# Optimization experiments

Measured on AMD Instinct MI355X. Metric: run time of the kernel, lower is better.

Reference implementation:

```python
import jax, jax.numpy as jnp
import numpy as np

B, S, D, H, F = 64, 512, 512, 512, 8
G = 4 * H // F  # 256, rows of left Kronecker factors


def setup_inputs() -> dict:
    key = jax.random.key(0)
    ks = jax.random.split(key, 24)

    def n(k, shape, s=0.05):
        return jax.random.normal(k, shape, jnp.float32) * s

    return {
        "x": jax.random.normal(ks[0], (B, S, D), jnp.float32),
        "h0": jnp.zeros((2, B, H), jnp.float32),
        "c0": jnp.zeros((2, B, H), jnp.float32),
        # layer 1 (input dim D)
        "W11": n(ks[1], (G, 1)), "W12": n(ks[2], (F, D)),
        "U11": n(ks[3], (G, 1)), "U12": n(ks[4], (F, H)),
        "dW11": n(ks[5], (G, 1)), "dW12": n(ks[6], (F, D)),
        "dU11": n(ks[7], (G, 1)), "dU12": n(ks[8], (F, H)),
        "b11": n(ks[9], (4 * H, 1)), "b12": n(ks[10], (4 * H, 1)),
        # layer 2 (input dim H; init_weights reshapes W22 to (F, H))
        "W21": n(ks[11], (G, 1)), "W22": n(ks[12], (F, H)),
        "U21": n(ks[13], (G, 1)), "U22": n(ks[14], (F, H)),
        "dW21": n(ks[15], (G, 1)), "dW22": n(ks[16], (F, H)),
        "dU21": n(ks[17], (G, 1)), "dU22": n(ks[18], (F, H)),
        "b21": n(ks[19], (4 * H, 1)), "b22": n(ks[20], (4 * H, 1)),
    }


def _kron_col(a, M):
    # kron of column vector a:(G,1) with M:(F,B) -> (G*F, B) = (4H, B)
    return (a[:, :, None] * M[None, :, :]).reshape(a.shape[0] * M.shape[0], M.shape[1])


def _cell(xt, ht, ct, p):
    # xt:(B,Din) ht,ct:(B,H); gates computed as (4H,B) like the torch code
    W1, W2, U1, U2, dW1, dW2, dU1, dU2, b1, b2 = p
    g = (_kron_col(W1, W2 @ xt.T) + _kron_col(dW1, dW2 @ xt.T)
         + _kron_col(U1, U2 @ ht.T) + _kron_col(dU1, dU2 @ ht.T)
         + b1 + b2)
    i = jax.nn.sigmoid(g[:H])
    f = jax.nn.sigmoid(g[H:2 * H])
    gg = jnp.tanh(g[2 * H:3 * H])
    o = jax.nn.sigmoid(g[3 * H:])
    c = f * ct.T + i * gg            # (H,B)
    h = o * jnp.tanh(c)              # (H,B)
    return h.T, c.T                  # (B,H)


def reference(x, h0, c0,
              W11, W12, U11, U12, dW11, dW12, dU11, dU12, b11, b12,
              W21, W22, U21, U22, dW21, dW22, dU21, dU22, b21, b22):
    layers = [
        (W11, W12, U11, U12, dW11, dW12, dU11, dU12, b11, b12),
        (W21, W22, U21, U22, dW21, dW22, dU21, dU22, b21, b22),
    ]

    def step(carry, xt):
        h, c = carry  # each (2,B,H)
        inp = xt
        hs, cs = [], []
        for li in range(2):
            hn, cn = _cell(inp, h[li], c[li], layers[li])
            hs.append(hn)
            cs.append(cn)
            inp = hn
        return (jnp.stack(hs), jnp.stack(cs)), inp

    (hn, cn), seq = jax.lax.scan(step, (h0, c0), jnp.swapaxes(x, 0, 1))
    hidden_seq = jnp.swapaxes(seq, 0, 1)  # (B,S,H)
    return hidden_seq, hn, cn
```

## Files before the change

### kernel.cpp

```cpp
#include <hip/hip_runtime.h>
#include <math.h>

#define NB 64
#define NS 512
#define ND 512
#define NH 512
#define L2E 1.4426950408889634f

__device__ __forceinline__ float dpp_sum64(float x) {
    x += __int_as_float(__builtin_amdgcn_update_dpp(0, __float_as_int(x), 0x111, 0xf, 0xf, true));
    x += __int_as_float(__builtin_amdgcn_update_dpp(0, __float_as_int(x), 0x112, 0xf, 0xf, true));
    x += __int_as_float(__builtin_amdgcn_update_dpp(0, __float_as_int(x), 0x114, 0xf, 0xf, true));
    x += __int_as_float(__builtin_amdgcn_update_dpp(0, __float_as_int(x), 0x118, 0xf, 0xf, true));
    x += __int_as_float(__builtin_amdgcn_update_dpp(0, __float_as_int(x), 0x142, 0xa, 0xf, true));
    x += __int_as_float(__builtin_amdgcn_update_dpp(0, __float_as_int(x), 0x143, 0xc, 0xf, true));
    return x;
}

__device__ __forceinline__ float bcast63(float x) {
    return __int_as_float(__builtin_amdgcn_readlane(__float_as_int(x), 63));
}
__device__ __forceinline__ float rcp_fast(float x) { return __builtin_amdgcn_rcpf(x); }
__device__ __forceinline__ float exp2_fast(float x) {
    float r;
    asm("v_exp_f32 %0, %1" : "=v"(r) : "v"(x));
    return r;
}
__device__ __forceinline__ void wg_barrier() {
    asm volatile("s_waitcnt lgkmcnt(0)\n\ts_barrier" ::: "memory");
}

__device__ __forceinline__ float dot8s(const float* s, float4 x0, float4 x1) {
    float r = s[0] * x0.x;
    r = fmaf(s[1], x0.y, r); r = fmaf(s[2], x0.z, r); r = fmaf(s[3], x0.w, r);
    r = fmaf(s[4], x1.x, r); r = fmaf(s[5], x1.y, r); r = fmaf(s[6], x1.z, r);
    r = fmaf(s[7], x1.w, r);
    return r;
}

#define LW(mat, f, arr)                                                       \
    {                                                                         \
        const float* M = (mat) + (f) * NH;                                    \
        arr[0] = M[kb];      arr[1] = M[kb + 8];                              \
        arr[2] = M[kb + 16]; arr[3] = M[kb + 24];                             \
        arr[4] = M[kb + 4];  arr[5] = M[kb + 12];                             \
        arr[6] = M[kb + 20]; arr[7] = M[kb + 28];                             \
    }

#define GATEX(t1, t2, m3, m4, bb, cS, hS)                                     \
    {                                                                         \
        float g0 = fmaf(cw[0], (t1), fmaf(cdw[0], (t2), fmaf(cu[0], (m3), fmaf(cdu[0], (m4), bb[0])))); \
        float g1 = fmaf(cw[1], (t1), fmaf(cdw[1], (t2), fmaf(cu[1], (m3), fmaf(cdu[1], (m4), bb[1])))); \
        float g2 = fmaf(cw[2], (t1), fmaf(cdw[2], (t2), fmaf(cu[2], (m3), fmaf(cdu[2], (m4), bb[2])))); \
        float g3 = fmaf(cw[3], (t1), fmaf(cdw[3], (t2), fmaf(cu[3], (m3), fmaf(cdu[3], (m4), bb[3])))); \
        float ig = rcp_fast(1.0f + exp2_fast(g0));                            \
        float fg = rcp_fast(1.0f + exp2_fast(g1));                            \
        float gg = fmaf(-2.0f, rcp_fast(1.0f + exp2_fast(g2)), 1.0f);         \
        float og = rcp_fast(1.0f + exp2_fast(g3));                            \
        cS = fmaf(fg, cS, ig * gg);                                           \
        hS = og * fmaf(-2.0f, rcp_fast(1.0f + exp2_fast(cS * (2.0f * L2E))), 1.0f); \
    }

__global__ __launch_bounds__(64) void precomp_kernel(
    const float* __restrict__ x, const float* __restrict__ W12,
    const float* __restrict__ dW12, float* __restrict__ PT) {
    int bt = blockIdx.x;
    int l = threadIdx.x;
    const float4* xr = (const float4*)(x + (size_t)bt * ND);
    float4 xv0 = xr[l];
    float4 xv1 = xr[64 + l];

    float acc[16];
#pragma unroll
    for (int f = 0; f < 8; ++f) {
        const float4* w = (const float4*)(W12 + f * ND);
        float4 a = w[l], b = w[64 + l];
        float s = a.x * xv0.x;
        s = fmaf(a.y, xv0.y, s); s = fmaf(a.z, xv0.z, s); s = fmaf(a.w, xv0.w, s);
        s = fmaf(b.x, xv1.x, s); s = fmaf(b.y, xv1.y, s); s = fmaf(b.z, xv1.z, s);
        s = fmaf(b.w, xv1.w, s);
        acc[f] = s;
        const float4* dw = (const float4*)(dW12 + f * ND);
        float4 c = dw[l], d = dw[64 + l];
        float u = c.x * xv0.x;
        u = fmaf(c.y, xv0.y, u); u = fmaf(c.z, xv0.z, u); u = fmaf(c.w, xv0.w, u);
        u = fmaf(d.x, xv1.x, u); u = fmaf(d.y, xv1.y, u); u = fmaf(d.z, xv1.z, u);
        u = fmaf(d.w, xv1.w, u);
        acc[8 + f] = u;
    }
#pragma unroll
    for (int f = 0; f < 16; ++f) acc[f] = dpp_sum64(acc[f]);

    if (l == 63) {
        float2* o = (float2*)(PT + (size_t)bt * 16);
#pragma unroll
        for (int g = 0; g < 8; ++g) o[g] = make_float2(acc[g], acc[8 + g]);
    }
}

__global__ __launch_bounds__(1024, 4) void lstm_fused_kernel(
    const float* __restrict__ PT, const float* __restrict__ h0,
    const float* __restrict__ c0,
    const float* __restrict__ W11, const float* __restrict__ U11,
    const float* __restrict__ dW11, const float* __restrict__ dU11,
    const float* __restrict__ U12, const float* __restrict__ dU12,
    const float* __restrict__ b11, const float* __restrict__ b12,
    const float* __restrict__ W21, const float* __restrict__ U21,
    const float* __restrict__ dW21, const float* __restrict__ dU21,
    const float* __restrict__ W22, const float* __restrict__ dW22,
    const float* __restrict__ U22, const float* __restrict__ dU22,
    const float* __restrict__ b21, const float* __restrict__ b22,
    float* __restrict__ out) {
    int b = blockIdx.x;
    int tid = threadIdx.x;
    int wv = tid >> 6;
    int l = tid & 63;
    int g = wv & 7;
    int kb = 32 * (l & 15) + (l >> 4);
    int r = 8 * l + g;

    __shared__ float Ps[NS * 16];
    __shared__ float hb1[2][NH];
    __shared__ float hb2[2][NH];
    __shared__ float mr[2][16];

    {
        const float4* src = (const float4*)(PT + (size_t)b * NS * 16);
        float4* dst = (float4*)Ps;
        dst[tid] = src[tid];
        dst[tid + 1024] = src[tid + 1024];
    }

    float* hn = out + (size_t)NB * NS * NH;
    float* cn = hn + (size_t)2 * NB * NH;
    const float SQ[4] = {-L2E, -L2E, 2.0f * L2E, -L2E};

    if (wv < 8) {
        float wU[8], wD[8], wW[8], wV[8];
        LW(U12, g, wU)
        LW(dU12, g, wD)
        LW(W22, g, wW)
        LW(dW22, g, wV)

        float cw[4], cdw[4], cu[4], cdu[4], bb[4];
#pragma unroll
        for (int q = 0; q < 4; ++q) {
            cw[q] = W11[q * 64 + l] * SQ[q];
            cdw[q] = dW11[q * 64 + l] * SQ[q];
            cu[q] = U11[q * 64 + l] * SQ[q];
            cdu[q] = dU11[q * 64 + l] * SQ[q];
            bb[q] = (b11[q * NH + r] + b12[q * NH + r]) * SQ[q];
        }
        float hA = h0[(size_t)b * NH + r];
        float cA = c0[(size_t)b * NH + r];
        hb1[0][64 * g + l] = hA;
        wg_barrier();

        for (int i = 0; i <= NS + 1; ++i) {
            if (i <= NS) {
                float4 x0 = *(const float4*)&hb1[i & 1][4 * l];
                float4 x1 = *(const float4*)&hb1[i & 1][256 + 4 * l];
                float rW = dpp_sum64(dot8s(wW, x0, x1));
                float rV = dpp_sum64(dot8s(wV, x0, x1));
                if (i > 0 && l == 63)
                    *(float2*)&mr[(i - 1) & 1][2 * g] = make_float2(rW, rV);
                if (i < NS) {
                    float rU = dpp_sum64(dot8s(wU, x0, x1));
                    float rD = dpp_sum64(dot8s(wD, x0, x1));
                    float m3 = bcast63(rU), m4 = bcast63(rD);
                    float2 pv = *(const float2*)&Ps[i * 16 + 2 * g];
                    GATEX(pv.x, pv.y, m3, m4, bb, cA, hA)
                    hb1[(i + 1) & 1][64 * g + l] = hA;
                }
            }
            wg_barrier();
        }
        hn[(size_t)b * NH + r] = hA;
        cn[(size_t)b * NH + r] = cA;
    } else {
        float wU[8], wD[8];
        LW(U22, g, wU)
        LW(dU22, g, wD)

        float cw[4], cdw[4], cu[4], cdu[4], bb[4];
#pragma unroll
        for (int q = 0; q < 4; ++q) {
            cw[q] = W21[q * 64 + l] * SQ[q];
            cdw[q] = dW21[q * 64 + l] * SQ[q];
            cu[q] = U21[q * 64 + l] * SQ[q];
            cdu[q] = dU21[q * 64 + l] * SQ[q];
            bb[q] = (b21[q * NH + r] + b22[q * NH + r]) * SQ[q];
        }
        float hA = h0[(size_t)NB * NH + (size_t)b * NH + r];
        float cA = c0[(size_t)NB * NH + (size_t)b * NH + r];
        hb2[0][64 * g + l] = hA;
        wg_barrier();

        float* outb = out + (size_t)b * NS * NH;
        for (int i = 0; i <= NS + 1; ++i) {
            int s = i - 2;
            if (s >= 0) {
                float4 y0 = *(const float4*)&hb2[s & 1][4 * l];
                float4 y1 = *(const float4*)&hb2[s & 1][256 + 4 * l];
                float rU = dpp_sum64(dot8s(wU, y0, y1));
                float rD = dpp_sum64(dot8s(wD, y0, y1));
                float m5 = bcast63(rU), m6 = bcast63(rD);
                float2 mv = *(const float2*)&mr[s & 1][2 * g];
                GATEX(mv.x, mv.y, m5, m6, bb, cA, hA)
                hb2[(s + 1) & 1][64 * g + l] = hA;
                outb[(size_t)s * NH + r] = hA;
            }
            wg_barrier();
        }
        hn[(size_t)NB * NH + (size_t)b * NH + r] = hA;
        cn[(size_t)NB * NH + (size_t)b * NH + r] = cA;
    }
}

extern "C" void kernel_launch(void* const* d_in, const int* in_sizes, int n_in,
                              void* d_out, int out_size, void* d_ws, size_t ws_size,
                              hipStream_t stream) {
    const float* x = (const float*)d_in[0];
    const float* h0 = (const float*)d_in[1];
    const float* c0 = (const float*)d_in[2];
    const float* W11 = (const float*)d_in[3];
    const float* W12 = (const float*)d_in[4];
    const float* U11 = (const float*)d_in[5];
    const float* U12 = (const float*)d_in[6];
    const float* dW11 = (const float*)d_in[7];
    const float* dW12 = (const float*)d_in[8];
    const float* dU11 = (const float*)d_in[9];
    const float* dU12 = (const float*)d_in[10];
    const float* b11 = (const float*)d_in[11];
    const float* b12 = (const float*)d_in[12];
    const float* W21 = (const float*)d_in[13];
    const float* W22 = (const float*)d_in[14];
    const float* U21 = (const float*)d_in[15];
    const float* U22 = (const float*)d_in[16];
    const float* dW21 = (const float*)d_in[17];
    const float* dW22 = (const float*)d_in[18];
    const float* dU21 = (const float*)d_in[19];
    const float* dU22 = (const float*)d_in[20];
    const float* b21 = (const float*)d_in[21];
    const float* b22 = (const float*)d_in[22];

    float* PT = (float*)d_ws;
    float* out = (float*)d_out;

    hipLaunchKernelGGL(precomp_kernel, dim3(NB * NS), dim3(64), 0, stream,
                       x, W12, dW12, PT);
    hipLaunchKernelGGL(lstm_fused_kernel, dim3(NB), dim3(1024), 0, stream,
                       PT, h0, c0,
                       W11, U11, dW11, dU11, U12, dU12, b11, b12,
                       W21, U21, dW21, dU21, W22, dW22, U22, dU22, b21, b22,
                       out);
}
```

Baseline: 430.8 us.

## Split LSTM layers into separate workgroups pipelined via global flags

Layer 1 and layer 2 now run in separate 512-thread workgroups (128 blocks total) instead of one 1024-thread block per batch row. Layer 1 writes its projected inputs for layer 2 to a global buffer and releases a flag every 8 steps, and layer 2 spins on these flags and consumes chunks of 8 steps. This decouples the two recurrences so each block only barriers its own 8 waves, aiming to shorten per-step barrier cost. It adds global memory traffic, spin-wait latency, a memset, and relies on both roles being co-resident to avoid deadlock.

```diff
diff --git a/kernel.cpp b/kernel.cpp
--- a/kernel.cpp
+++ b/kernel.cpp
@@ -5,6 +5,7 @@
 #define NS 512
 #define ND 512
 #define NH 512
+#define NC (NS / 8)
 #define L2E 1.4426950408889634f
 
 __device__ __forceinline__ float dpp_sum64(float x) {
@@ -28,6 +29,15 @@
 }
 __device__ __forceinline__ void wg_barrier() {
     asm volatile("s_waitcnt lgkmcnt(0)\n\ts_barrier" ::: "memory");
+}
+__device__ __forceinline__ void full_barrier() {
+    asm volatile("s_waitcnt vmcnt(0) lgkmcnt(0)\n\ts_barrier" ::: "memory");
+}
+__device__ __forceinline__ void spin_on(const unsigned int* p) {
+    while (__hip_atomic_load(p, __ATOMIC_ACQUIRE, __HIP_MEMORY_SCOPE_AGENT) == 0) {}
+}
+__device__ __forceinline__ void release_flag(unsigned int* p) {
+    __hip_atomic_store(p, 1u, __ATOMIC_RELEASE, __HIP_MEMORY_SCOPE_AGENT);
 }
 
 __device__ __forceinline__ float dot8s(const float* s, float4 x0, float4 x1) {
@@ -98,7 +108,7 @@
     }
 }
 
-__global__ __launch_bounds__(1024, 4) void lstm_fused_kernel(
+__global__ __launch_bounds__(512, 2) void lstm_pipe_kernel(
     const float* __restrict__ PT, const float* __restrict__ h0,
     const float* __restrict__ c0,
     const float* __restrict__ W11, const float* __restrict__ U11,
@@ -110,32 +120,31 @@
     const float* __restrict__ W22, const float* __restrict__ dW22,
     const float* __restrict__ U22, const float* __restrict__ dU22,
     const float* __restrict__ b21, const float* __restrict__ b22,
+    float* __restrict__ mrecT, unsigned int* __restrict__ flagb,
     float* __restrict__ out) {
-    int b = blockIdx.x;
+    int role = blockIdx.x >> 6;
+    int b = blockIdx.x & 63;
     int tid = threadIdx.x;
     int wv = tid >> 6;
     int l = tid & 63;
-    int g = wv & 7;
+    int g = wv;
     int kb = 32 * (l & 15) + (l >> 4);
     int r = 8 * l + g;
 
     __shared__ float Ps[NS * 16];
-    __shared__ float hb1[2][NH];
-    __shared__ float hb2[2][NH];
-    __shared__ float mr[2][16];
-
-    {
-        const float4* src = (const float4*)(PT + (size_t)b * NS * 16);
-        float4* dst = (float4*)Ps;
-        dst[tid] = src[tid];
-        dst[tid + 1024] = src[tid + 1024];
-    }
+    __shared__ float hb[2][NH];
 
     float* hn = out + (size_t)NB * NS * NH;
     float* cn = hn + (size_t)2 * NB * NH;
     const float SQ[4] = {-L2E, -L2E, 2.0f * L2E, -L2E};
 
-    if (wv < 8) {
+    if (role == 0) {
+        {
+            const float4* src = (const float4*)(PT + (size_t)b * NS * 16);
+            float4* dst = (float4*)Ps;
+#pragma unroll
+            for (int i = 0; i < 4; ++i) dst[tid + i * 512] = src[tid + i * 512];
+        }
         float wU[8], wD[8], wW[8], wV[8];
         LW(U12, g, wU)
         LW(dU12, g, wD)
@@ -153,27 +162,35 @@
         }
         float hA = h0[(size_t)b * NH + r];
         float cA = c0[(size_t)b * NH + r];
-        hb1[0][64 * g + l] = hA;
+        hb[0][tid] = hA;
         wg_barrier();
 
-        for (int i = 0; i <= NS + 1; ++i) {
-            if (i <= NS) {
-                float4 x0 = *(const float4*)&hb1[i & 1][4 * l];
-                float4 x1 = *(const float4*)&hb1[i & 1][256 + 4 * l];
-                float rW = dpp_sum64(dot8s(wW, x0, x1));
-                float rV = dpp_sum64(dot8s(wV, x0, x1));
-                if (i > 0 && l == 63)
-                    *(float2*)&mr[(i - 1) & 1][2 * g] = make_float2(rW, rV);
-                if (i < NS) {
-                    float rU = dpp_sum64(dot8s(wU, x0, x1));
-                    float rD = dpp_sum64(dot8s(wD, x0, x1));
-                    float m3 = bcast63(rU), m4 = bcast63(rD);
-                    float2 pv = *(const float2*)&Ps[i * 16 + 2 * g];
-                    GATEX(pv.x, pv.y, m3, m4, bb, cA, hA)
-                    hb1[(i + 1) & 1][64 * g + l] = hA;
-                }
-            }
-            wg_barrier();
+        unsigned int* fb = flagb + b * NC;
+        for (int i = 0; i <= NS; ++i) {
+            float4 x0 = *(const float4*)&hb[i & 1][4 * l];
+            float4 x1 = *(const float4*)&hb[i & 1][256 + 4 * l];
+            float rW = dpp_sum64(dot8s(wW, x0, x1));
+            float rV = dpp_sum64(dot8s(wV, x0, x1));
+            if (i > 0 && l == 63) {
+                int s = i - 1;
+                float* rec = mrecT +
+                    ((size_t)(b * NC + (s >> 3)) * 8 + g) * 16 + 2 * (s & 7);
+                *(float2*)rec = make_float2(rW, rV);
+            }
+            if (i < NS) {
+                float rU = dpp_sum64(dot8s(wU, x0, x1));
+                float rD = dpp_sum64(dot8s(wD, x0, x1));
+                float m3 = bcast63(rU), m4 = bcast63(rD);
+                float2 pv = *(const float2*)&Ps[i * 16 + 2 * g];
+                GATEX(pv.x, pv.y, m3, m4, bb, cA, hA)
+                hb[(i + 1) & 1][tid] = hA;
+            }
+            if ((i & 7) == 0 && i > 0) {
+                full_barrier();
+                if (tid == 0) release_flag(&fb[(i >> 3) - 1]);
+            } else {
+                wg_barrier();
+            }
         }
         hn[(size_t)b * NH + r] = hA;
         cn[(size_t)b * NH + r] = cA;
@@ -193,24 +210,31 @@
         }
         float hA = h0[(size_t)NB * NH + (size_t)b * NH + r];
         float cA = c0[(size_t)NB * NH + (size_t)b * NH + r];
-        hb2[0][64 * g + l] = hA;
+        hb[0][tid] = hA;
         wg_barrier();
 
+        const unsigned int* fb = flagb + b * NC;
         float* outb = out + (size_t)b * NS * NH;
-        for (int i = 0; i <= NS + 1; ++i) {
-            int s = i - 2;
-            if (s >= 0) {
-                float4 y0 = *(const float4*)&hb2[s & 1][4 * l];
-                float4 y1 = *(const float4*)&hb2[s & 1][256 + 4 * l];
+        for (int k = 0; k < NC; ++k) {
+            spin_on(&fb[k]);
+            const float4* rec = (const float4*)(mrecT +
+                ((size_t)(b * NC + k) * 8 + g) * 16);
+            float4 q0 = rec[0], q1 = rec[1], q2 = rec[2], q3 = rec[3];
+            float mq[16] = {q0.x, q0.y, q0.z, q0.w, q1.x, q1.y, q1.z, q1.w,
+                            q2.x, q2.y, q2.z, q2.w, q3.x, q3.y, q3.z, q3.w};
+#pragma unroll
+            for (int j = 0; j < 8; ++j) {
+                int s = k * 8 + j;
+                float4 y0 = *(const float4*)&hb[s & 1][4 * l];
+                float4 y1 = *(const float4*)&hb[s & 1][256 + 4 * l];
                 float rU = dpp_sum64(dot8s(wU, y0, y1));
                 float rD = dpp_sum64(dot8s(wD, y0, y1));
                 float m5 = bcast63(rU), m6 = bcast63(rD);
-                float2 mv = *(const float2*)&mr[s & 1][2 * g];
-                GATEX(mv.x, mv.y, m5, m6, bb, cA, hA)
-                hb2[(s + 1) & 1][64 * g + l] = hA;
+                GATEX(mq[2 * j], mq[2 * j + 1], m5, m6, bb, cA, hA)
+                hb[(s + 1) & 1][tid] = hA;
                 outb[(size_t)s * NH + r] = hA;
-            }
-            wg_barrier();
+                wg_barrier();
+            }
         }
         hn[(size_t)NB * NH + (size_t)b * NH + r] = hA;
         cn[(size_t)NB * NH + (size_t)b * NH + r] = cA;
@@ -244,14 +268,18 @@
     const float* b21 = (const float*)d_in[21];
     const float* b22 = (const float*)d_in[22];
 
-    float* PT = (float*)d_ws;
+    char* ws = (char*)d_ws;
+    float* PT = (float*)ws;
+    float* mrecT = (float*)(ws + (size_t)2 * 1024 * 1024);
+    unsigned int* flagb = (unsigned int*)(ws + (size_t)4 * 1024 * 1024);
     float* out = (float*)d_out;
 
+    hipMemsetAsync(flagb, 0, NB * NC * sizeof(unsigned int), stream);
     hipLaunchKernelGGL(precomp_kernel, dim3(NB * NS), dim3(64), 0, stream,
                        x, W12, dW12, PT);
-    hipLaunchKernelGGL(lstm_fused_kernel, dim3(NB), dim3(1024), 0, stream,
+    hipLaunchKernelGGL(lstm_pipe_kernel, dim3(2 * NB), dim3(512), 0, stream,
                        PT, h0, c0,
                        W11, U11, dW11, dU11, U12, dU12, b11, b12,
                        W21, U21, dW21, dU21, W22, dW22, U22, dU22, b21, b22,
-                       out);
-}
+                       mrecT, flagb, out);
+}
```

Result: slower. 480.2 us (+11.5%).
